# Kernel optimization log

Measured on AMD Instinct MI355X. Metric: run time of the kernel, lower is better.

Reference implementation:

```python
import jax, jax.numpy as jnp
import numpy as np

B, S, T, D, H_HEADS = 2, 2048, 2048, 1024, 16
HD = D // H_HEADS
EPS = 1e-5


def _ln(x, g, b):
    m = jnp.mean(x, axis=-1, keepdims=True)
    v = jnp.mean(jnp.square(x - m), axis=-1, keepdims=True)
    return g * (x - m) * jax.lax.rsqrt(v + EPS) + b


def _mha(xq, xkv, Wq, bq, Wk, bk, Wv, bv, Wo, bo, causal):
    Bq, Lq, _ = xq.shape
    Lk = xkv.shape[1]
    q = (xq @ Wq + bq).reshape(Bq, Lq, H_HEADS, HD)
    k = (xkv @ Wk + bk).reshape(Bq, Lk, H_HEADS, HD)
    v = (xkv @ Wv + bv).reshape(Bq, Lk, H_HEADS, HD)
    scores = jnp.einsum('bqhd,bkhd->bhqk', q, k) / jnp.sqrt(jnp.asarray(HD, q.dtype))
    if causal:
        mask = jnp.tril(jnp.ones((Lq, Lk), dtype=bool))
        scores = jnp.where(mask, scores, jnp.asarray(-1e9, scores.dtype))
    p = jax.nn.softmax(scores, axis=-1)
    o = jnp.einsum('bhqk,bkhd->bqhd', p, v).reshape(Bq, Lq, D)
    return o @ Wo + bo


def setup_inputs() -> dict:
    key = jax.random.key(0)
    ks = jax.random.split(key, 24)
    s = 0.02
    def w(i):
        return jax.random.normal(ks[i], (D, D), jnp.float32) * s
    inp = {
        'S0': jax.random.normal(ks[20], (B, S, D), jnp.float32),
        'H': jax.random.normal(ks[21], (B, T, D), jnp.float32),
        'Wq1': w(0), 'bq1': jnp.zeros((D,)), 'Wk1': w(1), 'bk1': jnp.zeros((D,)),
        'Wv1': w(2), 'bv1': jnp.zeros((D,)), 'Wo1': w(3), 'bo1': jnp.zeros((D,)),
        'ln1_g': jnp.ones((D,)), 'ln1_b': jnp.zeros((D,)),
        'Wq2': w(4), 'bq2': jnp.zeros((D,)), 'Wk2': w(5), 'bk2': jnp.zeros((D,)),
        'Wv2': w(6), 'bv2': jnp.zeros((D,)), 'Wo2': w(7), 'bo2': jnp.zeros((D,)),
        'ln2_g': jnp.ones((D,)), 'ln2_b': jnp.zeros((D,)),
        'Wf': w(8), 'bf': jnp.zeros((D,)),
        'ln3_g': jnp.ones((D,)), 'ln3_b': jnp.zeros((D,)),
    }
    return inp


def reference(S0, H, Wq1, bq1, Wk1, bk1, Wv1, bv1, Wo1, bo1, ln1_g, ln1_b,
              Wq2, bq2, Wk2, bk2, Wv2, bv2, Wo2, bo2, ln2_g, ln2_b,
              Wf, bf, ln3_g, ln3_b):
    # masked (causal) self-attention + add&norm
    a1 = _mha(S0, S0, Wq1, bq1, Wk1, bk1, Wv1, bv1, Wo1, bo1, causal=True)
    S1 = _ln(S0 + a1, ln1_g, ln1_b)
    # cross-attention over encoder output H + add&norm
    a2 = _mha(S1, H, Wq2, bq2, Wk2, bk2, Wv2, bv2, Wo2, bo2, causal=False)
    S2 = _ln(S1 + a2, ln2_g, ln2_b)
    # FFN (single Linear) + add&norm
    S3 = _ln(S2 + (S2 @ Wf + bf), ln3_g, ln3_b)
    return S3
```

## Files before the change

### kernel.cpp

```cpp
#include <hip/hip_runtime.h>
#include <hip/hip_bf16.h>
#include <cstdint>
#include <cstddef>


#define D_DIM 1024
#define SEQ   2048
#define NHEAD 16
#define HDIM  64
#define MROWS 4096

typedef __attribute__((ext_vector_type(8)))  short bf16x8;
typedef __attribute__((ext_vector_type(4)))  float f32x4;
typedef __attribute__((ext_vector_type(16))) float f32x16;
typedef __attribute__((ext_vector_type(4)))  unsigned int u32x4;

static __device__ __forceinline__ short f2bf(float x) {
    __hip_bfloat16 h = __float2bfloat16(x);
    return *reinterpret_cast<short*>(&h);
}

static __device__ __forceinline__ unsigned int cvtpk(float lo, float hi2) {
    unsigned int r;
    asm("v_cvt_pk_bf16_f32 %0, %1, %2" : "=v"(r) : "v"(lo), "v"(hi2));
    return r;
}

#define GLOAD_LDS16(g, l)                                                     \
    __builtin_amdgcn_global_load_lds(                                         \
        (const __attribute__((address_space(1))) unsigned int*)(g),           \
        (__attribute__((address_space(3))) unsigned int*)(l), 16, 0, 0)

struct WPtrs { const float* p[9]; };

__global__ __launch_bounds__(256) void prep_kernel(
    WPtrs wp, short* __restrict__ Wt,
    const float* __restrict__ s0, const float* __restrict__ hx,
    short* __restrict__ d0, short* __restrict__ d1,
    const float* __restrict__ bq1, const float* __restrict__ bk1,
    const float* __restrict__ bv1, const float* __restrict__ bk2,
    const float* __restrict__ bv2, float* __restrict__ cb1,
    float* __restrict__ cb2)
{
    __shared__ float tl[64][65];
    const int t = threadIdx.x;
    const int id = blockIdx.x;
    if (id < 2304) {
        const int z = id >> 8, rem = id & 255;
        const float* src = wp.p[z];
        short* dst = Wt + (size_t)z * D_DIM * D_DIM;
        const int r0 = (rem >> 4) * 64;
        const int c0 = (rem & 15) * 64;
        #pragma unroll
        for (int i = 0; i < 4; ++i) {
            int row = i * 16 + (t >> 4);
            int col = (t & 15) * 4;
            float4 v = *(const float4*)(src + (size_t)(r0 + row) * D_DIM + c0 + col);
            tl[row][col + 0] = v.x; tl[row][col + 1] = v.y;
            tl[row][col + 2] = v.z; tl[row][col + 3] = v.w;
        }
        __syncthreads();
        #pragma unroll
        for (int i = 0; i < 4; ++i) {
            int nrow = i * 16 + (t >> 4);
            int kcol = (t & 15) * 4;
            ushort4 o;
            o.x = (unsigned short)f2bf(tl[kcol + 0][nrow]);
            o.y = (unsigned short)f2bf(tl[kcol + 1][nrow]);
            o.z = (unsigned short)f2bf(tl[kcol + 2][nrow]);
            o.w = (unsigned short)f2bf(tl[kcol + 3][nrow]);
            *(ushort4*)(dst + (size_t)(c0 + nrow) * D_DIM + r0 + kcol) = o;
        }
    } else if (id < 6400) {
        const int cid = id - 2304;
        const bool second = cid >= 2048;
        const float* src = second ? hx : s0;
        short* dst = second ? d1 : d0;
        size_t i = ((size_t)(cid - (second ? 2048 : 0)) * 256 + t) * 8;
        float4 a = *(const float4*)(src + i);
        float4 b = *(const float4*)(src + i + 4);
        bf16x8 o;
        o[0] = f2bf(a.x); o[1] = f2bf(a.y); o[2] = f2bf(a.z); o[3] = f2bf(a.w);
        o[4] = f2bf(b.x); o[5] = f2bf(b.y); o[6] = f2bf(b.z); o[7] = f2bf(b.w);
        *(bf16x8*)(dst + i) = o;
    } else {
        const int i = (id - 6400) * 256 + t;
        if      (i < 1024) cb1[i] = bq1[i];
        else if (i < 2048) cb1[i] = bk1[i - 1024];
        else if (i < 3072) cb1[i] = bv1[i - 2048];
        else if (i < 4096) cb2[i - 3072] = bk2[i - 3072];
        else               cb2[i - 3072] = bv2[i - 4096];
    }
}

__device__ __forceinline__ void gemm_qkv_body(
    short* __restrict__ As_, short* __restrict__ Bs_,
    const short* __restrict__ A, const short* __restrict__ Bt,
    const float* __restrict__ bias,
    short* __restrict__ Qh, short* __restrict__ Kh, short* __restrict__ Vh,
    int col0, float qscale, int bx, int by)
{
    const int t = threadIdx.x;
    const int wave = t >> 6, lane = t & 63;
    const int wm = wave >> 1, wn = wave & 1;
    const int m0 = bx * 128, n0 = by * 128;
    const int l15 = lane & 15, l4 = lane >> 4;
    const int lrow = lane >> 2, lcol = (lane & 3) * 8;
    f32x4 acc[4][4] = {};
    for (int k0 = 0; k0 < D_DIM; k0 += 32) {
        __syncthreads();
        #pragma unroll
        for (int c = 0; c < 2; ++c) {
            int chunk = wave + c * 4;
            int row = chunk * 16 + lrow;
            GLOAD_LDS16(A  + (size_t)(m0 + row) * D_DIM + k0 + lcol,
                        As_ + chunk * 512 + lane * 8);
            GLOAD_LDS16(Bt + (size_t)(n0 + row) * D_DIM + k0 + lcol,
                        Bs_ + chunk * 512 + lane * 8);
        }
        __syncthreads();
        bf16x8 af[4], bfr[4];
        const int kq = l4 * 8;
        #pragma unroll
        for (int i = 0; i < 4; ++i)
            af[i] = *(const bf16x8*)&As_[(wm * 64 + i * 16 + l15) * 32 + kq];
        #pragma unroll
        for (int j = 0; j < 4; ++j)
            bfr[j] = *(const bf16x8*)&Bs_[(wn * 64 + j * 16 + l15) * 32 + kq];
        #pragma unroll
        for (int i = 0; i < 4; ++i)
            #pragma unroll
            for (int j = 0; j < 4; ++j)
                acc[i][j] = __builtin_amdgcn_mfma_f32_16x16x32_bf16(
                    af[i], bfr[j], acc[i][j], 0, 0, 0);
    }
    const int rbase = m0 + wm * 64;
    const int cbase = n0 + wn * 64;
    float bv[4];
    #pragma unroll
    for (int j = 0; j < 4; ++j) bv[j] = bias[cbase + j * 16 + l15];
    #pragma unroll
    for (int i = 0; i < 4; ++i) {
        #pragma unroll
        for (int r = 0; r < 4; ++r) {
            const int grow = rbase + i * 16 + l4 * 4 + r;
            const int b = grow >> 11, s = grow & 2047;
            #pragma unroll
            for (int j = 0; j < 4; ++j) {
                const int vcol = col0 + cbase + j * 16 + l15;
                float v = acc[i][j][r] + bv[j];
                if (vcol < 1024) v *= qscale;
                short* dst = (vcol < 1024) ? Qh : ((vcol < 2048) ? Kh : Vh);
                const int h = (vcol >> 6) & 15, hd = vcol & 63;
                dst[((size_t)(b * 16 + h) * SEQ + s) * HDIM + hd] = f2bf(v);
            }
        }
    }
}

__global__ __launch_bounds__(256) void gemm_qkv_kernel(
    const short* __restrict__ A, const short* __restrict__ Bt,
    const float* __restrict__ bias,
    short* __restrict__ Qh, short* __restrict__ Kh, short* __restrict__ Vh,
    int col0, float qscale)
{
    __shared__ short lds[8192];
    gemm_qkv_body(lds, lds + 4096, A, Bt, bias, Qh, Kh, Vh,
                  col0, qscale, blockIdx.x, blockIdx.y);
}

__global__ __launch_bounds__(256) void gemm_resid_kernel(
    const short* __restrict__ A, const short* __restrict__ Bt,
    const float* __restrict__ bias, const float* __restrict__ resid,
    float* __restrict__ Cout)
{
    __shared__ short As[128 * 32];
    __shared__ short Bs[64 * 32];
    const int t = threadIdx.x;
    const int wave = t >> 6, lane = t & 63;
    const int wm = wave >> 1, wn = wave & 1;
    const int m0 = blockIdx.x * 128, n0 = blockIdx.y * 64;
    const int l15 = lane & 15, l4 = lane >> 4;
    const int lrow = lane >> 2, lcol = (lane & 3) * 8;
    f32x4 acc[4][2] = {};
    for (int k0 = 0; k0 < D_DIM; k0 += 32) {
        __syncthreads();
        #pragma unroll
        for (int c = 0; c < 2; ++c) {
            int chunk = wave + c * 4;
            int row = chunk * 16 + lrow;
            GLOAD_LDS16(A + (size_t)(m0 + row) * D_DIM + k0 + lcol,
                        As + chunk * 512 + lane * 8);
        }
        {
            int row = wave * 16 + lrow;
            GLOAD_LDS16(Bt + (size_t)(n0 + row) * D_DIM + k0 + lcol,
                        Bs + wave * 512 + lane * 8);
        }
        __syncthreads();
        bf16x8 af[4], bfr[2];
        const int kq = l4 * 8;
        #pragma unroll
        for (int i = 0; i < 4; ++i)
            af[i] = *(const bf16x8*)&As[(wm * 64 + i * 16 + l15) * 32 + kq];
        #pragma unroll
        for (int j = 0; j < 2; ++j)
            bfr[j] = *(const bf16x8*)&Bs[(wn * 32 + j * 16 + l15) * 32 + kq];
        #pragma unroll
        for (int i = 0; i < 4; ++i)
            #pragma unroll
            for (int j = 0; j < 2; ++j)
                acc[i][j] = __builtin_amdgcn_mfma_f32_16x16x32_bf16(
                    af[i], bfr[j], acc[i][j], 0, 0, 0);
    }
    const int rbase = m0 + wm * 64;
    const int cbase = n0 + wn * 32;
    float bv[2];
    #pragma unroll
    for (int j = 0; j < 2; ++j) bv[j] = bias[cbase + j * 16 + l15];
    #pragma unroll
    for (int i = 0; i < 4; ++i) {
        #pragma unroll
        for (int r = 0; r < 4; ++r) {
            const int grow = rbase + i * 16 + l4 * 4 + r;
            #pragma unroll
            for (int j = 0; j < 2; ++j) {
                const int gcol = cbase + j * 16 + l15;
                float v = acc[i][j][r] + bv[j]
                        + resid[(size_t)grow * D_DIM + gcol];
                Cout[(size_t)grow * D_DIM + gcol] = v;
            }
        }
    }
}

__global__ __launch_bounds__(256) void gemm_q_kernel(
    const short* __restrict__ A, const short* __restrict__ Bt,
    const float* __restrict__ bias, short* __restrict__ Qh, float qscale)
{
    __shared__ short As[128 * 32];
    __shared__ short Bs[64 * 32];
    const int t = threadIdx.x;
    const int wave = t >> 6, lane = t & 63;
    const int wm = wave >> 1, wn = wave & 1;
    const int m0 = blockIdx.x * 128, n0 = blockIdx.y * 64;
    const int l15 = lane & 15, l4 = lane >> 4;
    const int lrow = lane >> 2, lcol = (lane & 3) * 8;
    f32x4 acc[4][2] = {};
    for (int k0 = 0; k0 < D_DIM; k0 += 32) {
        __syncthreads();
        #pragma unroll
        for (int c = 0; c < 2; ++c) {
            int chunk = wave + c * 4;
            int row = chunk * 16 + lrow;
            GLOAD_LDS16(A + (size_t)(m0 + row) * D_DIM + k0 + lcol,
                        As + chunk * 512 + lane * 8);
        }
        {
            int row = wave * 16 + lrow;
            GLOAD_LDS16(Bt + (size_t)(n0 + row) * D_DIM + k0 + lcol,
                        Bs + wave * 512 + lane * 8);
        }
        __syncthreads();
        bf16x8 af[4], bfr[2];
        const int kq = l4 * 8;
        #pragma unroll
        for (int i = 0; i < 4; ++i)
            af[i] = *(const bf16x8*)&As[(wm * 64 + i * 16 + l15) * 32 + kq];
        #pragma unroll
        for (int j = 0; j < 2; ++j)
            bfr[j] = *(const bf16x8*)&Bs[(wn * 32 + j * 16 + l15) * 32 + kq];
        #pragma unroll
        for (int i = 0; i < 4; ++i)
            #pragma unroll
            for (int j = 0; j < 2; ++j)
                acc[i][j] = __builtin_amdgcn_mfma_f32_16x16x32_bf16(
                    af[i], bfr[j], acc[i][j], 0, 0, 0);
    }
    const int rbase = m0 + wm * 64;
    const int cbase = n0 + wn * 32;
    float bv[2];
    #pragma unroll
    for (int j = 0; j < 2; ++j) bv[j] = bias[cbase + j * 16 + l15];
    #pragma unroll
    for (int i = 0; i < 4; ++i) {
        #pragma unroll
        for (int r = 0; r < 4; ++r) {
            const int grow = rbase + i * 16 + l4 * 4 + r;
            const int b = grow >> 11, s = grow & 2047;
            #pragma unroll
            for (int j = 0; j < 2; ++j) {
                const int vcol = cbase + j * 16 + l15;
                const float v = (acc[i][j][r] + bv[j]) * qscale;
                const int h = (vcol >> 6) & 15, hd = vcol & 63;
                Qh[((size_t)(b * 16 + h) * SEQ + s) * HDIM + hd] = f2bf(v);
            }
        }
    }
}

template<bool CAUSAL, bool VSINGLE>
__device__ __forceinline__ void attn_body(
    char* ldsb,
    const short* __restrict__ Qh, const short* __restrict__ Kh,
    const short* __restrict__ Vh, short* __restrict__ O, const int id)
{
    const int t = threadIdx.x, wave = t >> 6, lane = t & 63;
    const int q_own = lane & 31, hi = lane >> 5;
    const int bh = ((id & 7) << 2) | ((id >> 3) & 3);
    const int qsel = id >> 5;
    const int b = bh >> 4, h = bh & 15;
    const short* Qp = Qh + (size_t)bh * SEQ * HDIM;
    const short* Kp = Kh + (size_t)bh * SEQ * HDIM;
    const short* Vp = Vh + (size_t)bh * SEQ * HDIM;
    short* Op = O + (size_t)b * SEQ * D_DIM + h * HDIM;

    const int ksrc = (t & 7) ^ ((t >> 3) & 7);
    const int vr2 = (t & 31) * 2, vg = (t >> 5) * 8;
    const int swz = (q_own & 7) << 3;

    bf16x8 ones;
    #pragma unroll
    for (int j = 0; j < 8; ++j) ones[j] = (short)0x3F80;

    const int npm = CAUSAL ? 2 : 1;
    for (int pm = 0; pm < npm; ++pm) {
        const int qt = CAUSAL ? (pm == 0 ? qsel : 15 - qsel) : qsel;
        const int q0 = qt * 128;
        const int qw = q0 + wave * 32;

        bf16x8 qf[4];
        #pragma unroll
        for (int s = 0; s < 4; ++s)
            qf[s] = *(const bf16x8*)(Qp + (size_t)(qw + q_own) * HDIM
                                     + s * 16 + hi * 8);

        int qkb[4], pvb[8], vwb[8], kgb;
        #pragma unroll
        for (int s = 0; s < 4; ++s)
            qkb[s] = q_own * 128 + 2 * ((s * 16 + hi * 8) ^ swz);
        #pragma unroll
        for (int ks = 0; ks < 8; ++ks)
            pvb[ks] = 32768 + q_own * 256 + 2 * ((ks * 16 + hi * 8) ^ swz);
        #pragma unroll
        for (int j = 0; j < 8; ++j)
            vwb[j] = 32768 + (vg + j) * 256 + 2 * (vr2 ^ (j << 3));
        kgb = t * 16;

        f32x16 oacc[2] = {};
        f32x16 lsum = {};
        float m_ = 0.0f;
        const int nkt = CAUSAL ? (qt + 1) : (SEQ / 128);

        bf16x8 va0, vb0, va1, vb1;

        if (pm) __syncthreads();

        #pragma unroll
        for (int c = 0; c < 4; ++c) {
            const int row = c * 32 + (t >> 3);
            GLOAD_LDS16(Kp + (size_t)row * HDIM + ksrc * 8,
                        ldsb + kgb + c * 4096);
        }
        va0 = *(const bf16x8*)(Vp + (size_t)vr2 * HDIM + vg);
        vb0 = *(const bf16x8*)(Vp + (size_t)(vr2 + 1) * HDIM + vg);
        va1 = *(const bf16x8*)(Vp + (size_t)(64 + vr2) * HDIM + vg);
        vb1 = *(const bf16x8*)(Vp + (size_t)(65 + vr2) * HDIM + vg);
        #pragma unroll
        for (int j = 0; j < 8; ++j) {
            unsigned int p0 = ((unsigned int)(unsigned short)vb0[j] << 16)
                            | (unsigned short)va0[j];
            unsigned int p1 = ((unsigned int)(unsigned short)vb1[j] << 16)
                            | (unsigned short)va1[j];
            *(unsigned int*)(ldsb + vwb[j])       = p0;
            *(unsigned int*)(ldsb + vwb[j] + 128) = p1;
        }
        __syncthreads();
        kgb ^= 16384;
        if (!VSINGLE) {
            #pragma unroll
            for (int j = 0; j < 8; ++j) vwb[j] ^= 16384;
        }

        for (int kt = 0; kt < nkt; ++kt) {
            const int kbase = kt * 128;
            const bool have_next = (kt + 1 < nkt);

            if (have_next) {
                #pragma unroll
                for (int c = 0; c < 4; ++c) {
                    const int row = kbase + 128 + c * 32 + (t >> 3);
                    GLOAD_LDS16(Kp + (size_t)row * HDIM + ksrc * 8,
                                ldsb + kgb + c * 4096);
                }
                va0 = *(const bf16x8*)(Vp + (size_t)(kbase + 128 + vr2) * HDIM + vg);
                vb0 = *(const bf16x8*)(Vp + (size_t)(kbase + 129 + vr2) * HDIM + vg);
                va1 = *(const bf16x8*)(Vp + (size_t)(kbase + 192 + vr2) * HDIM + vg);
                vb1 = *(const bf16x8*)(Vp + (size_t)(kbase + 193 + vr2) * HDIM + vg);
            }

            f32x16 minit;
            #pragma unroll
            for (int rr = 0; rr < 16; ++rr) minit[rr] = -m_;
            f32x16 sc[4];
            sc[0] = minit; sc[1] = minit; sc[2] = minit; sc[3] = minit;
            __builtin_amdgcn_s_setprio(1);
            #pragma unroll
            for (int kt2 = 0; kt2 < 4; ++kt2) {
                #pragma unroll
                for (int s = 0; s < 4; ++s) {
                    bf16x8 kf = *(const bf16x8*)(ldsb + qkb[s] + kt2 * 4096);
                    sc[kt2] = __builtin_amdgcn_mfma_f32_32x32x16_bf16(
                        kf, qf[s], sc[kt2], 0, 0, 0);
                }
            }
            __builtin_amdgcn_s_setprio(0);

            if (CAUSAL && (kbase + 127 > qw)) {
                #pragma unroll
                for (int kt2 = 0; kt2 < 4; ++kt2)
                    #pragma unroll
                    for (int rr = 0; rr < 16; ++rr) {
                        const int k = kbase + kt2 * 32
                                    + (rr & 3) + 8 * (rr >> 2) + 4 * hi;
                        if (k > qw + q_own) sc[kt2][rr] = -1e30f;
                    }
            }

            float km[4];
            #pragma unroll
            for (int kt2 = 0; kt2 < 4; ++kt2) {
                float t0 = fmaxf(fmaxf(sc[kt2][0],  sc[kt2][1]),  sc[kt2][2]);
                float t1 = fmaxf(fmaxf(sc[kt2][3],  sc[kt2][4]),  sc[kt2][5]);
                float t2 = fmaxf(fmaxf(sc[kt2][6],  sc[kt2][7]),  sc[kt2][8]);
                float t3 = fmaxf(fmaxf(sc[kt2][9],  sc[kt2][10]), sc[kt2][11]);
                float t4 = fmaxf(fmaxf(sc[kt2][12], sc[kt2][13]), sc[kt2][14]);
                float u  = fmaxf(fmaxf(t0, t1), t2);
                float v  = fmaxf(fmaxf(t3, t4), sc[kt2][15]);
                km[kt2] = fmaxf(u, v);
            }
            float smax = fmaxf(fmaxf(fmaxf(km[0], km[1]), km[2]), km[3]);
            smax = fmaxf(smax, __shfl_xor(smax, 32));

            if (!__all(smax <= 8.0f)) {
                const float sp = fmaxf(smax, 0.f);
                const float corr = exp2f(-sp);
                lsum[0] *= corr;
                #pragma unroll
                for (int ht = 0; ht < 2; ++ht)
                    #pragma unroll
                    for (int rr = 0; rr < 16; ++rr)
                        oacc[ht][rr] *= corr;
                #pragma unroll
                for (int kt2 = 0; kt2 < 4; ++kt2)
                    #pragma unroll
                    for (int rr = 0; rr < 16; ++rr)
                        sc[kt2][rr] -= sp;
                m_ += sp;
            }

            #pragma unroll
            for (int kt2 = 0; kt2 < 4; ++kt2)
                #pragma unroll
                for (int rr = 0; rr < 16; ++rr)
                    sc[kt2][rr] = exp2f(sc[kt2][rr]);

            u32x4 paw[8];
            #pragma unroll
            for (int kt2 = 0; kt2 < 4; ++kt2) {
                unsigned int w0a = cvtpk(sc[kt2][0],  sc[kt2][1]);
                unsigned int w0b = cvtpk(sc[kt2][2],  sc[kt2][3]);
                unsigned int w1a = cvtpk(sc[kt2][4],  sc[kt2][5]);
                unsigned int w1b = cvtpk(sc[kt2][6],  sc[kt2][7]);
                unsigned int w2a = cvtpk(sc[kt2][8],  sc[kt2][9]);
                unsigned int w2b = cvtpk(sc[kt2][10], sc[kt2][11]);
                unsigned int w3a = cvtpk(sc[kt2][12], sc[kt2][13]);
                unsigned int w3b = cvtpk(sc[kt2][14], sc[kt2][15]);
                asm("v_permlane32_swap_b32 %0, %1" : "+v"(w0a), "+v"(w1a));
                asm("v_permlane32_swap_b32 %0, %1" : "+v"(w0b), "+v"(w1b));
                asm("v_permlane32_swap_b32 %0, %1" : "+v"(w2a), "+v"(w3a));
                asm("v_permlane32_swap_b32 %0, %1" : "+v"(w2b), "+v"(w3b));
                paw[kt2 * 2 + 0][0] = w0a; paw[kt2 * 2 + 0][1] = w0b;
                paw[kt2 * 2 + 0][2] = w1a; paw[kt2 * 2 + 0][3] = w1b;
                paw[kt2 * 2 + 1][0] = w2a; paw[kt2 * 2 + 1][1] = w2b;
                paw[kt2 * 2 + 1][2] = w3a; paw[kt2 * 2 + 1][3] = w3b;
            }

            __builtin_amdgcn_s_setprio(1);
            #pragma unroll
            for (int ks = 0; ks < 8; ++ks) {
                union { u32x4 u; bf16x8 bv8; } pc;
                pc.u = paw[ks];
                bf16x8 vf0 = *(const bf16x8*)(ldsb + pvb[ks]);
                oacc[0] = __builtin_amdgcn_mfma_f32_32x32x16_bf16(
                    vf0, pc.bv8, oacc[0], 0, 0, 0);
                bf16x8 vf1 = *(const bf16x8*)(ldsb + pvb[ks] + 8192);
                oacc[1] = __builtin_amdgcn_mfma_f32_32x32x16_bf16(
                    vf1, pc.bv8, oacc[1], 0, 0, 0);
                lsum = __builtin_amdgcn_mfma_f32_32x32x16_bf16(
                    ones, pc.bv8, lsum, 0, 0, 0);
            }
            __builtin_amdgcn_s_setprio(0);

            if (have_next) {
                if (VSINGLE) {
                    __syncthreads();
                    #pragma unroll
                    for (int j = 0; j < 8; ++j) {
                        unsigned int p0 = ((unsigned int)(unsigned short)vb0[j] << 16)
                                        | (unsigned short)va0[j];
                        unsigned int p1 = ((unsigned int)(unsigned short)vb1[j] << 16)
                                        | (unsigned short)va1[j];
                        *(unsigned int*)(ldsb + vwb[j])       = p0;
                        *(unsigned int*)(ldsb + vwb[j] + 128) = p1;
                    }
                    __syncthreads();
                } else {
                    #pragma unroll
                    for (int j = 0; j < 8; ++j) {
                        unsigned int p0 = ((unsigned int)(unsigned short)vb0[j] << 16)
                                        | (unsigned short)va0[j];
                        unsigned int p1 = ((unsigned int)(unsigned short)vb1[j] << 16)
                                        | (unsigned short)va1[j];
                        *(unsigned int*)(ldsb + vwb[j])       = p0;
                        *(unsigned int*)(ldsb + vwb[j] + 128) = p1;
                    }
                    __syncthreads();
                }
            }
            kgb ^= 16384;
            #pragma unroll
            for (int s = 0; s < 4; ++s) qkb[s] ^= 16384;
            if (!VSINGLE) {
                #pragma unroll
                for (int ks = 0; ks < 8; ++ks) pvb[ks] ^= 16384;
                #pragma unroll
                for (int j = 0; j < 8; ++j) vwb[j] ^= 16384;
            }
        }

        const float inv = 1.0f / lsum[0];
        const int grow = qw + q_own;
        #pragma unroll
        for (int ht = 0; ht < 2; ++ht)
            #pragma unroll
            for (int j = 0; j < 4; ++j) {
                ushort4 o;
                o.x = (unsigned short)f2bf(oacc[ht][4 * j + 0] * inv);
                o.y = (unsigned short)f2bf(oacc[ht][4 * j + 1] * inv);
                o.z = (unsigned short)f2bf(oacc[ht][4 * j + 2] * inv);
                o.w = (unsigned short)f2bf(oacc[ht][4 * j + 3] * inv);
                *(ushort4*)&Op[(size_t)grow * D_DIM + ht * 32 + 8 * j + 4 * hi] = o;
            }
    }
}

template<bool CAUSAL>
__global__ __launch_bounds__(256, 2) void attn_mfma_kernel(
    const short* __restrict__ Qh, const short* __restrict__ Kh,
    const short* __restrict__ Vh, short* __restrict__ O)
{
    __shared__ short lds[32768];
    attn_body<CAUSAL, false>((char*)lds, Qh, Kh, Vh, O, blockIdx.x);
}

__global__ __launch_bounds__(256, 2) void fused_cattn_kv2_kernel(
    const short* __restrict__ Qh, const short* __restrict__ Kh,
    const short* __restrict__ Vh, short* __restrict__ O,
    const short* __restrict__ A2, const short* __restrict__ Bt2,
    const float* __restrict__ bias2,
    short* __restrict__ Kh2, short* __restrict__ Vh2)
{
    __shared__ short lds[24576];
    if (blockIdx.x < 256) {
        attn_body<true, true>((char*)lds, Qh, Kh, Vh, O, blockIdx.x);
    } else {
        const int bx2 = blockIdx.x - 256;
        gemm_qkv_body(lds, lds + 4096, A2, Bt2, bias2,
                      nullptr, Kh2, Vh2, 1024, 1.0f, bx2 & 31, bx2 >> 5);
    }
}

__global__ __launch_bounds__(256) void ln_kernel(
    const float* __restrict__ X, const float* __restrict__ g,
    const float* __restrict__ bb, float* __restrict__ outf,
    short* __restrict__ outb)
{
    const int row = blockIdx.x;
    const int t = threadIdx.x;
    const float* x = X + (size_t)row * D_DIM;
    float4 v = *(const float4*)(x + (t << 2));
    float s  = v.x + v.y + v.z + v.w;
    float sq = v.x * v.x + v.y * v.y + v.z * v.z + v.w * v.w;
    #pragma unroll
    for (int off = 1; off < 64; off <<= 1) {
        s  += __shfl_xor(s, off);
        sq += __shfl_xor(sq, off);
    }
    __shared__ float ss[4], ssq[4];
    const int wid = t >> 6, lane = t & 63;
    if (lane == 0) { ss[wid] = s; ssq[wid] = sq; }
    __syncthreads();
    s  = ss[0] + ss[1] + ss[2] + ss[3];
    sq = ssq[0] + ssq[1] + ssq[2] + ssq[3];
    const float mean = s * (1.0f / 1024.0f);
    const float var  = sq * (1.0f / 1024.0f) - mean * mean;
    const float inv  = rsqrtf(var + 1e-5f);
    float4 gv = *(const float4*)(g  + (t << 2));
    float4 bv = *(const float4*)(bb + (t << 2));
    float4 o;
    o.x = gv.x * (v.x - mean) * inv + bv.x;
    o.y = gv.y * (v.y - mean) * inv + bv.y;
    o.z = gv.z * (v.z - mean) * inv + bv.z;
    o.w = gv.w * (v.w - mean) * inv + bv.w;
    if (outf) *(float4*)(outf + (size_t)row * D_DIM + (t << 2)) = o;
    if (outb) {
        ushort4 ob;
        ob.x = (unsigned short)f2bf(o.x); ob.y = (unsigned short)f2bf(o.y);
        ob.z = (unsigned short)f2bf(o.z); ob.w = (unsigned short)f2bf(o.w);
        *(ushort4*)(outb + (size_t)row * D_DIM + (t << 2)) = ob;
    }
}

extern "C" void kernel_launch(void* const* d_in, const int* in_sizes, int n_in,
                              void* d_out, int out_size, void* d_ws, size_t ws_size,
                              hipStream_t stream)
{
    (void)in_sizes; (void)n_in; (void)out_size; (void)ws_size;
    const float* S0f = (const float*)d_in[0];
    const float* Hf  = (const float*)d_in[1];
    const float* bq1 = (const float*)d_in[3];
    const float* bk1 = (const float*)d_in[5];
    const float* bv1 = (const float*)d_in[7];
    const float* bo1 = (const float*)d_in[9];
    const float* g1  = (const float*)d_in[10]; const float* b1 = (const float*)d_in[11];
    const float* bq2 = (const float*)d_in[13];
    const float* bk2 = (const float*)d_in[15];
    const float* bv2 = (const float*)d_in[17];
    const float* bo2 = (const float*)d_in[19];
    const float* g2  = (const float*)d_in[20]; const float* b2 = (const float*)d_in[21];
    const float* bff = (const float*)d_in[23];
    const float* g3  = (const float*)d_in[24]; const float* b3 = (const float*)d_in[25];

    char* ws = (char*)d_ws;
    size_t off = 0;
    auto alloc = [&](size_t bytes) { char* p = ws + off; off += (bytes + 255) & ~(size_t)255; return p; };
    short* Wt   = (short*)alloc((size_t)9 * D_DIM * D_DIM * 2);
    short* bS0  = (short*)alloc((size_t)MROWS * D_DIM * 2);
    short* bH   = (short*)alloc((size_t)MROWS * D_DIM * 2);
    short* Qhb  = (short*)alloc((size_t)MROWS * D_DIM * 2);
    short* Khb  = (short*)alloc((size_t)MROWS * D_DIM * 2);
    short* Vhb  = (short*)alloc((size_t)MROWS * D_DIM * 2);
    short* Khb2 = (short*)alloc((size_t)MROWS * D_DIM * 2);
    short* Vhb2 = (short*)alloc((size_t)MROWS * D_DIM * 2);
    short* bAO  = (short*)alloc((size_t)MROWS * D_DIM * 2);
    float* X    = (float*)alloc((size_t)MROWS * D_DIM * 4);
    short* bSx  = (short*)alloc((size_t)MROWS * D_DIM * 2);
    float* cb1  = (float*)alloc(3072 * 4);
    float* cb2  = (float*)alloc(2048 * 4);

    const size_t WSTRIDE = (size_t)D_DIM * D_DIM;
    const float QSCALE = 0.125f * 1.44269504088896f;

    WPtrs wp;
    wp.p[0] = (const float*)d_in[2];
    wp.p[1] = (const float*)d_in[4];
    wp.p[2] = (const float*)d_in[6];
    wp.p[3] = (const float*)d_in[8];
    wp.p[4] = (const float*)d_in[12];
    wp.p[5] = (const float*)d_in[14];
    wp.p[6] = (const float*)d_in[16];
    wp.p[7] = (const float*)d_in[18];
    wp.p[8] = (const float*)d_in[22];

    prep_kernel<<<dim3(6420), 256, 0, stream>>>(
        wp, Wt, S0f, Hf, bS0, bH, bq1, bk1, bv1, bk2, bv2, cb1, cb2);

    const dim3 blk(256);
    const dim3 attn_grid_f(512);
    const dim3 resid_grid(32, 16);

    gemm_qkv_kernel<<<dim3(32, 24), blk, 0, stream>>>(
        bS0, Wt, cb1, Qhb, Khb, Vhb, 0, QSCALE);
    fused_cattn_kv2_kernel<<<dim3(768), blk, 0, stream>>>(
        Qhb, Khb, Vhb, bAO, bH, Wt + 5 * WSTRIDE, cb2, Khb2, Vhb2);
    gemm_resid_kernel<<<resid_grid, blk, 0, stream>>>(
        bAO, Wt + 3 * WSTRIDE, bo1, S0f, X);
    ln_kernel<<<MROWS, blk, 0, stream>>>(X, g1, b1, X, bSx);

    gemm_q_kernel<<<resid_grid, blk, 0, stream>>>(
        bSx, Wt + 4 * WSTRIDE, bq2, Qhb, QSCALE);
    attn_mfma_kernel<false><<<attn_grid_f, blk, 0, stream>>>(
        Qhb, Khb2, Vhb2, bAO);
    gemm_resid_kernel<<<resid_grid, blk, 0, stream>>>(
        bAO, Wt + 7 * WSTRIDE, bo2, X, X);
    ln_kernel<<<MROWS, blk, 0, stream>>>(X, g2, b2, X, bSx);

    gemm_resid_kernel<<<resid_grid, blk, 0, stream>>>(
        bSx, Wt + 8 * WSTRIDE, bff, X, X);
    ln_kernel<<<MROWS, blk, 0, stream>>>(X, g3, b3, (float*)d_out, nullptr);
}
```

Measured before the change: 267.8 us.

## Split cross-attention over KV halves with a separate combine kernel

Replaces the single non-causal attention launch with a split-KV kernel. Each block handles one of two 1024-key halves, doubling the grid from 512 to 1024 blocks, and writes unnormalized fp32 partial outputs plus row sum and max. A combine kernel then merges the halves with rescaling into bf16. The partials reuse dead workspace buffers, and the split kernel drops to a smaller LDS footprint with single V buffering. This gains occupancy and parallelism at the cost of extra fp32 traffic and one more launch.

```diff
diff --git a/kernel.cpp b/kernel.cpp
--- a/kernel.cpp
+++ b/kernel.cpp
@@ -32,6 +32,7 @@
         (__attribute__((address_space(3))) unsigned int*)(l), 16, 0, 0)
 
 struct WPtrs { const float* p[9]; };
+struct OPtrs { float* p[4]; };
 
 __global__ __launch_bounds__(256) void prep_kernel(
     WPtrs wp, short* __restrict__ Wt,
@@ -503,30 +504,17 @@
             __builtin_amdgcn_s_setprio(0);
 
             if (have_next) {
-                if (VSINGLE) {
-                    __syncthreads();
-                    #pragma unroll
-                    for (int j = 0; j < 8; ++j) {
-                        unsigned int p0 = ((unsigned int)(unsigned short)vb0[j] << 16)
-                                        | (unsigned short)va0[j];
-                        unsigned int p1 = ((unsigned int)(unsigned short)vb1[j] << 16)
-                                        | (unsigned short)va1[j];
-                        *(unsigned int*)(ldsb + vwb[j])       = p0;
-                        *(unsigned int*)(ldsb + vwb[j] + 128) = p1;
-                    }
-                    __syncthreads();
-                } else {
-                    #pragma unroll
-                    for (int j = 0; j < 8; ++j) {
-                        unsigned int p0 = ((unsigned int)(unsigned short)vb0[j] << 16)
-                                        | (unsigned short)va0[j];
-                        unsigned int p1 = ((unsigned int)(unsigned short)vb1[j] << 16)
-                                        | (unsigned short)va1[j];
-                        *(unsigned int*)(ldsb + vwb[j])       = p0;
-                        *(unsigned int*)(ldsb + vwb[j] + 128) = p1;
-                    }
-                    __syncthreads();
+                if (VSINGLE) __syncthreads();
+                #pragma unroll
+                for (int j = 0; j < 8; ++j) {
+                    unsigned int p0 = ((unsigned int)(unsigned short)vb0[j] << 16)
+                                    | (unsigned short)va0[j];
+                    unsigned int p1 = ((unsigned int)(unsigned short)vb1[j] << 16)
+                                    | (unsigned short)va1[j];
+                    *(unsigned int*)(ldsb + vwb[j])       = p0;
+                    *(unsigned int*)(ldsb + vwb[j] + 128) = p1;
                 }
+                __syncthreads();
             }
             kgb ^= 16384;
             #pragma unroll
@@ -555,13 +543,252 @@
     }
 }
 
-template<bool CAUSAL>
-__global__ __launch_bounds__(256, 2) void attn_mfma_kernel(
+__global__ __launch_bounds__(256, 2) void attn_split_kernel(
     const short* __restrict__ Qh, const short* __restrict__ Kh,
-    const short* __restrict__ Vh, short* __restrict__ O)
-{
-    __shared__ short lds[32768];
-    attn_body<CAUSAL, false>((char*)lds, Qh, Kh, Vh, O, blockIdx.x);
+    const short* __restrict__ Vh, OPtrs op, float* __restrict__ LM)
+{
+    __shared__ short lds[24576];
+    char* ldsb = (char*)lds;
+    const int t = threadIdx.x, wave = t >> 6, lane = t & 63;
+    const int q_own = lane & 31, hi = lane >> 5;
+    const int id = blockIdx.x;
+    const int bh = ((id & 7) << 2) | ((id >> 3) & 3);
+    const int rest = id >> 5;
+    const int qt = rest & 15, sp = rest >> 4;
+    const short* Qp = Qh + (size_t)bh * SEQ * HDIM;
+    const short* Kp = Kh + (size_t)bh * SEQ * HDIM;
+    const short* Vp = Vh + (size_t)bh * SEQ * HDIM;
+
+    const int ksrc = (t & 7) ^ ((t >> 3) & 7);
+    const int vr2 = (t & 31) * 2, vg = (t >> 5) * 8;
+    const int swz = (q_own & 7) << 3;
+    const int kv0 = sp * 1024;
+
+    bf16x8 ones;
+    #pragma unroll
+    for (int j = 0; j < 8; ++j) ones[j] = (short)0x3F80;
+
+    const int qw = qt * 128 + wave * 32;
+    bf16x8 qf[4];
+    #pragma unroll
+    for (int s = 0; s < 4; ++s)
+        qf[s] = *(const bf16x8*)(Qp + (size_t)(qw + q_own) * HDIM
+                                 + s * 16 + hi * 8);
+
+    int qkb[4], pvb[8], vwb[8], kgb;
+    #pragma unroll
+    for (int s = 0; s < 4; ++s)
+        qkb[s] = q_own * 128 + 2 * ((s * 16 + hi * 8) ^ swz);
+    #pragma unroll
+    for (int ks = 0; ks < 8; ++ks)
+        pvb[ks] = 32768 + q_own * 256 + 2 * ((ks * 16 + hi * 8) ^ swz);
+    #pragma unroll
+    for (int j = 0; j < 8; ++j)
+        vwb[j] = 32768 + (vg + j) * 256 + 2 * (vr2 ^ (j << 3));
+    kgb = t * 16;
+
+    f32x16 oacc[2] = {};
+    f32x16 lsum = {};
+    float m_ = 0.0f;
+
+    bf16x8 va0, vb0, va1, vb1;
+
+    #pragma unroll
+    for (int c = 0; c < 4; ++c) {
+        const int row = kv0 + c * 32 + (t >> 3);
+        GLOAD_LDS16(Kp + (size_t)row * HDIM + ksrc * 8, ldsb + kgb + c * 4096);
+    }
+    va0 = *(const bf16x8*)(Vp + (size_t)(kv0 + vr2) * HDIM + vg);
+    vb0 = *(const bf16x8*)(Vp + (size_t)(kv0 + vr2 + 1) * HDIM + vg);
+    va1 = *(const bf16x8*)(Vp + (size_t)(kv0 + 64 + vr2) * HDIM + vg);
+    vb1 = *(const bf16x8*)(Vp + (size_t)(kv0 + 65 + vr2) * HDIM + vg);
+    #pragma unroll
+    for (int j = 0; j < 8; ++j) {
+        unsigned int p0 = ((unsigned int)(unsigned short)vb0[j] << 16)
+                        | (unsigned short)va0[j];
+        unsigned int p1 = ((unsigned int)(unsigned short)vb1[j] << 16)
+                        | (unsigned short)va1[j];
+        *(unsigned int*)(ldsb + vwb[j])       = p0;
+        *(unsigned int*)(ldsb + vwb[j] + 128) = p1;
+    }
+    __syncthreads();
+    kgb ^= 16384;
+
+    for (int kt = 0; kt < 8; ++kt) {
+        const int kbase = kv0 + kt * 128;
+        const bool have_next = (kt + 1 < 8);
+
+        if (have_next) {
+            #pragma unroll
+            for (int c = 0; c < 4; ++c) {
+                const int row = kbase + 128 + c * 32 + (t >> 3);
+                GLOAD_LDS16(Kp + (size_t)row * HDIM + ksrc * 8,
+                            ldsb + kgb + c * 4096);
+            }
+            va0 = *(const bf16x8*)(Vp + (size_t)(kbase + 128 + vr2) * HDIM + vg);
+            vb0 = *(const bf16x8*)(Vp + (size_t)(kbase + 129 + vr2) * HDIM + vg);
+            va1 = *(const bf16x8*)(Vp + (size_t)(kbase + 192 + vr2) * HDIM + vg);
+            vb1 = *(const bf16x8*)(Vp + (size_t)(kbase + 193 + vr2) * HDIM + vg);
+        }
+
+        f32x16 minit;
+        #pragma unroll
+        for (int rr = 0; rr < 16; ++rr) minit[rr] = -m_;
+        f32x16 sc[4];
+        sc[0] = minit; sc[1] = minit; sc[2] = minit; sc[3] = minit;
+        __builtin_amdgcn_s_setprio(1);
+        #pragma unroll
+        for (int kt2 = 0; kt2 < 4; ++kt2) {
+            #pragma unroll
+            for (int s = 0; s < 4; ++s) {
+                bf16x8 kf = *(const bf16x8*)(ldsb + qkb[s] + kt2 * 4096);
+                sc[kt2] = __builtin_amdgcn_mfma_f32_32x32x16_bf16(
+                    kf, qf[s], sc[kt2], 0, 0, 0);
+            }
+        }
+        __builtin_amdgcn_s_setprio(0);
+
+        float km[4];
+        #pragma unroll
+        for (int kt2 = 0; kt2 < 4; ++kt2) {
+            float t0 = fmaxf(fmaxf(sc[kt2][0],  sc[kt2][1]),  sc[kt2][2]);
+            float t1 = fmaxf(fmaxf(sc[kt2][3],  sc[kt2][4]),  sc[kt2][5]);
+            float t2 = fmaxf(fmaxf(sc[kt2][6],  sc[kt2][7]),  sc[kt2][8]);
+            float t3 = fmaxf(fmaxf(sc[kt2][9],  sc[kt2][10]), sc[kt2][11]);
+            float t4 = fmaxf(fmaxf(sc[kt2][12], sc[kt2][13]), sc[kt2][14]);
+            float u  = fmaxf(fmaxf(t0, t1), t2);
+            float v  = fmaxf(fmaxf(t3, t4), sc[kt2][15]);
+            km[kt2] = fmaxf(u, v);
+        }
+        float smax = fmaxf(fmaxf(fmaxf(km[0], km[1]), km[2]), km[3]);
+        smax = fmaxf(smax, __shfl_xor(smax, 32));
+
+        if (!__all(smax <= 8.0f)) {
+            const float spv = fmaxf(smax, 0.f);
+            const float corr = exp2f(-spv);
+            lsum[0] *= corr;
+            #pragma unroll
+            for (int ht = 0; ht < 2; ++ht)
+                #pragma unroll
+                for (int rr = 0; rr < 16; ++rr)
+                    oacc[ht][rr] *= corr;
+            #pragma unroll
+            for (int kt2 = 0; kt2 < 4; ++kt2)
+                #pragma unroll
+                for (int rr = 0; rr < 16; ++rr)
+                    sc[kt2][rr] -= spv;
+            m_ += spv;
+        }
+
+        #pragma unroll
+        for (int kt2 = 0; kt2 < 4; ++kt2)
+            #pragma unroll
+            for (int rr = 0; rr < 16; ++rr)
+                sc[kt2][rr] = exp2f(sc[kt2][rr]);
+
+        u32x4 paw[8];
+        #pragma unroll
+        for (int kt2 = 0; kt2 < 4; ++kt2) {
+            unsigned int w0a = cvtpk(sc[kt2][0],  sc[kt2][1]);
+            unsigned int w0b = cvtpk(sc[kt2][2],  sc[kt2][3]);
+            unsigned int w1a = cvtpk(sc[kt2][4],  sc[kt2][5]);
+            unsigned int w1b = cvtpk(sc[kt2][6],  sc[kt2][7]);
+            unsigned int w2a = cvtpk(sc[kt2][8],  sc[kt2][9]);
+            unsigned int w2b = cvtpk(sc[kt2][10], sc[kt2][11]);
+            unsigned int w3a = cvtpk(sc[kt2][12], sc[kt2][13]);
+            unsigned int w3b = cvtpk(sc[kt2][14], sc[kt2][15]);
+            asm("v_permlane32_swap_b32 %0, %1" : "+v"(w0a), "+v"(w1a));
+            asm("v_permlane32_swap_b32 %0, %1" : "+v"(w0b), "+v"(w1b));
+            asm("v_permlane32_swap_b32 %0, %1" : "+v"(w2a), "+v"(w3a));
+            asm("v_permlane32_swap_b32 %0, %1" : "+v"(w2b), "+v"(w3b));
+            paw[kt2 * 2 + 0][0] = w0a; paw[kt2 * 2 + 0][1] = w0b;
+            paw[kt2 * 2 + 0][2] = w1a; paw[kt2 * 2 + 0][3] = w1b;
+            paw[kt2 * 2 + 1][0] = w2a; paw[kt2 * 2 + 1][1] = w2b;
+            paw[kt2 * 2 + 1][2] = w3a; paw[kt2 * 2 + 1][3] = w3b;
+        }
+
+        __builtin_amdgcn_s_setprio(1);
+        #pragma unroll
+        for (int ks = 0; ks < 8; ++ks) {
+            union { u32x4 u; bf16x8 bv8; } pc;
+            pc.u = paw[ks];
+            bf16x8 vf0 = *(const bf16x8*)(ldsb + pvb[ks]);
+            oacc[0] = __builtin_amdgcn_mfma_f32_32x32x16_bf16(
+                vf0, pc.bv8, oacc[0], 0, 0, 0);
+            bf16x8 vf1 = *(const bf16x8*)(ldsb + pvb[ks] + 8192);
+            oacc[1] = __builtin_amdgcn_mfma_f32_32x32x16_bf16(
+                vf1, pc.bv8, oacc[1], 0, 0, 0);
+            lsum = __builtin_amdgcn_mfma_f32_32x32x16_bf16(
+                ones, pc.bv8, lsum, 0, 0, 0);
+        }
+        __builtin_amdgcn_s_setprio(0);
+
+        if (have_next) {
+            __syncthreads();
+            #pragma unroll
+            for (int j = 0; j < 8; ++j) {
+                unsigned int p0 = ((unsigned int)(unsigned short)vb0[j] << 16)
+                                | (unsigned short)va0[j];
+                unsigned int p1 = ((unsigned int)(unsigned short)vb1[j] << 16)
+                                | (unsigned short)va1[j];
+                *(unsigned int*)(ldsb + vwb[j])       = p0;
+                *(unsigned int*)(ldsb + vwb[j] + 128) = p1;
+            }
+            __syncthreads();
+        }
+        kgb ^= 16384;
+        #pragma unroll
+        for (int s = 0; s < 4; ++s) qkb[s] ^= 16384;
+    }
+
+    float* Osp = op.p[sp * 2 + (bh >> 4)]
+               + (size_t)(bh & 15) * SEQ * HDIM;
+    const int grow = qw + q_own;
+    #pragma unroll
+    for (int ht = 0; ht < 2; ++ht)
+        #pragma unroll
+        for (int j = 0; j < 4; ++j) {
+            float4 o4 = make_float4(oacc[ht][4 * j + 0], oacc[ht][4 * j + 1],
+                                    oacc[ht][4 * j + 2], oacc[ht][4 * j + 3]);
+            *(float4*)&Osp[(size_t)grow * HDIM + ht * 32 + 8 * j + 4 * hi] = o4;
+        }
+    if (hi == 0) {
+        float2 lm2 = make_float2(lsum[0], m_);
+        *(float2*)&LM[(((size_t)sp * 32 + bh) * SEQ + grow) * 2] = lm2;
+    }
+}
+
+__global__ __launch_bounds__(256) void attn_combine_kernel(
+    OPtrs op, const float* __restrict__ LM, short* __restrict__ O)
+{
+    const int idx = blockIdx.x * 256 + threadIdx.x;
+    const int hd8 = (idx & 7) * 8;
+    const int q   = (idx >> 3) & 2047;
+    const int bh  = idx >> 14;
+    const int b = bh >> 4, h = bh & 15;
+    const float2 lm1 = *(const float2*)&LM[(((size_t)0 * 32 + bh) * SEQ + q) * 2];
+    const float2 lm2 = *(const float2*)&LM[(((size_t)1 * 32 + bh) * SEQ + q) * 2];
+    const float m  = fmaxf(lm1.y, lm2.y);
+    const float w1 = exp2f(lm1.y - m), w2 = exp2f(lm2.y - m);
+    const float inv = 1.0f / (lm1.x * w1 + lm2.x * w2);
+    const float* O1 = op.p[0 + (bh >> 4)]
+                    + ((size_t)(bh & 15) * SEQ + q) * HDIM + hd8;
+    const float* O2 = op.p[2 + (bh >> 4)]
+                    + ((size_t)(bh & 15) * SEQ + q) * HDIM + hd8;
+    float4 a0 = *(const float4*)O1, a1 = *(const float4*)(O1 + 4);
+    float4 b0 = *(const float4*)O2, b1 = *(const float4*)(O2 + 4);
+    short* dst = O + ((size_t)b * SEQ + q) * D_DIM + h * HDIM + hd8;
+    ushort4 r0, r1;
+    r0.x = (unsigned short)f2bf((a0.x * w1 + b0.x * w2) * inv);
+    r0.y = (unsigned short)f2bf((a0.y * w1 + b0.y * w2) * inv);
+    r0.z = (unsigned short)f2bf((a0.z * w1 + b0.z * w2) * inv);
+    r0.w = (unsigned short)f2bf((a0.w * w1 + b0.w * w2) * inv);
+    r1.x = (unsigned short)f2bf((a1.x * w1 + b1.x * w2) * inv);
+    r1.y = (unsigned short)f2bf((a1.y * w1 + b1.y * w2) * inv);
+    r1.z = (unsigned short)f2bf((a1.z * w1 + b1.z * w2) * inv);
+    r1.w = (unsigned short)f2bf((a1.w * w1 + b1.w * w2) * inv);
+    *(ushort4*)dst       = r0;
+    *(ushort4*)(dst + 4) = r1;
 }
 
 __global__ __launch_bounds__(256, 2) void fused_cattn_kv2_kernel(
@@ -658,6 +885,7 @@
     short* bSx  = (short*)alloc((size_t)MROWS * D_DIM * 2);
     float* cb1  = (float*)alloc(3072 * 4);
     float* cb2  = (float*)alloc(2048 * 4);
+    float* LM   = (float*)alloc((size_t)2 * 32 * SEQ * 2 * 4);
 
     const size_t WSTRIDE = (size_t)D_DIM * D_DIM;
     const float QSCALE = 0.125f * 1.44269504088896f;
@@ -673,11 +901,16 @@
     wp.p[7] = (const float*)d_in[18];
     wp.p[8] = (const float*)d_in[22];
 
+    OPtrs op;
+    op.p[0] = (float*)bS0;
+    op.p[1] = (float*)bH;
+    op.p[2] = (float*)Khb;
+    op.p[3] = (float*)Vhb;
+
     prep_kernel<<<dim3(6420), 256, 0, stream>>>(
         wp, Wt, S0f, Hf, bS0, bH, bq1, bk1, bv1, bk2, bv2, cb1, cb2);
 
     const dim3 blk(256);
-    const dim3 attn_grid_f(512);
     const dim3 resid_grid(32, 16);
 
     gemm_qkv_kernel<<<dim3(32, 24), blk, 0, stream>>>(
@@ -690,8 +923,9 @@
 
     gemm_q_kernel<<<resid_grid, blk, 0, stream>>>(
         bSx, Wt + 4 * WSTRIDE, bq2, Qhb, QSCALE);
-    attn_mfma_kernel<false><<<attn_grid_f, blk, 0, stream>>>(
-        Qhb, Khb2, Vhb2, bAO);
+    attn_split_kernel<<<dim3(1024), blk, 0, stream>>>(
+        Qhb, Khb2, Vhb2, op, LM);
+    attn_combine_kernel<<<dim3(2048), blk, 0, stream>>>(op, LM, bAO);
     gemm_resid_kernel<<<resid_grid, blk, 0, stream>>>(
         bAO, Wt + 7 * WSTRIDE, bo2, X, X);
     ln_kernel<<<MROWS, blk, 0, stream>>>(X, g2, b2, X, bSx);
```

After: 277.4 us. 1.04x slower.
